# Kernel optimization log

Measured on AMD Instinct MI355X. Metric: run time of the kernel, lower is better.

The kernel has to match this reference:

```python
import jax, jax.numpy as jnp
import numpy as np

DT = 1e-3
STEPS = 128
UNITS_OSC = 512
MLP_UNITS = [1024, 512, 256]
ACTION_DIM = 256
BATCH = 64


def setup_inputs() -> dict:
    key = jax.random.key(0)
    ks = jax.random.split(key, 16)
    inp = {
        "z": jax.random.normal(ks[0], (BATCH, 2 * UNITS_OSC), dtype=jnp.float32),
        "omega": jax.random.uniform(ks[1], (BATCH, 1), dtype=jnp.float32),
        "b": jax.random.uniform(ks[2], (BATCH, UNITS_OSC), dtype=jnp.float32),
    }
    dims = [UNITS_OSC] + MLP_UNITS
    i = 3
    for l, (din, dout) in enumerate(zip(dims[:-1], dims[1:])):
        scale = 1.0 / np.sqrt(din)
        inp[f"W{l}_re"] = (jax.random.normal(ks[i], (din, dout), dtype=jnp.float32) * scale); i += 1
        inp[f"W{l}_im"] = (jax.random.normal(ks[i], (din, dout), dtype=jnp.float32) * scale); i += 1
        inp[f"b{l}_re"] = jnp.zeros((dout,), dtype=jnp.float32)
        inp[f"b{l}_im"] = jnp.zeros((dout,), dtype=jnp.float32)
    return inp


def _hopf(z, omega, b):
    # z: (B, 2*U) = [real | imag]; Hopf dynamics with harmonic frequencies k*omega
    x, y = z[:, :UNITS_OSC], z[:, UNITS_OSC:]
    r2 = x * x + y * y
    w = omega * jnp.arange(1, UNITS_OSC + 1, dtype=z.dtype)  # (B, U)
    dx = (b - r2) * x - w * y
    dy = (b - r2) * y + w * x
    return jnp.concatenate([x + DT * dx, y + DT * dy], axis=-1)


def _complex_mlp(z, params):
    # complex dense stack: (xr+i*yi) @ (Wr+i*Wi) + (br+i*bi), tanh on re/im parts
    x, y = jnp.split(z, 2, axis=-1)
    for (Wr, Wi, br, bi) in params:
        xr = x @ Wr - y @ Wi + br
        yi = x @ Wi + y @ Wr + bi
        x, y = jnp.tanh(xr), jnp.tanh(yi)
    return jnp.concatenate([x, y], axis=-1)


def reference(z, omega, b,
              W0_re, W0_im, b0_re, b0_im,
              W1_re, W1_im, b1_re, b1_im,
              W2_re, W2_im, b2_re, b2_im):
    params = [(W0_re, W0_im, b0_re, b0_im),
              (W1_re, W1_im, b1_re, b1_im),
              (W2_re, W2_im, b2_re, b2_im)]
    # first oscillator step (done before the while_loop in the original)
    z1 = _hopf(z, omega, b)
    o0 = _complex_mlp(z1, params)

    def step(zc, _):
        zn = _hopf(zc, omega, b)
        return zn, _complex_mlp(zn, params)

    _, outs = jax.lax.scan(step, z1, None, length=STEPS - 1)  # (STEPS-1, B, 2*A)
    outs = jnp.concatenate([o0[None], outs], axis=0)          # (STEPS, B, 2*A)
    out = jnp.transpose(outs, (1, 0, 2))[:, :, :ACTION_DIM]   # (B, STEPS, A)
    return out, z1
```

## Files before the change

kernel.cpp:

```cpp
#include <hip/hip_runtime.h>
#include <hip/hip_bf16.h>
#include <stdint.h>

#define AS1 __attribute__((address_space(1)))
#define AS3 __attribute__((address_space(3)))

typedef __bf16 bf16x8 __attribute__((ext_vector_type(8)));
typedef float f32x4 __attribute__((ext_vector_type(4)));

__device__ __forceinline__ float fast_tanh(float x) {
    float e = __expf(2.0f * x);
    return 1.0f - 2.0f / (e + 1.0f);
}

__device__ __forceinline__ float ldin(const void* p, int idx, int f32) {
    return f32 ? ((const float*)p)[idx]
               : __bfloat162float(((const __hip_bfloat16*)p)[idx]);
}

__device__ __forceinline__ unsigned short f2bf(float v) {
    __hip_bfloat16 h = __float2bfloat16(v);
    return *(unsigned short*)&h;
}

__device__ __forceinline__ void gload_lds16(const __hip_bfloat16* g, AS3 char* l) {
    __builtin_amdgcn_global_load_lds((AS1 void*)g, (AS3 void*)l, 16, 0, 0);
}

__device__ __forceinline__ void wt_tile(const void* Wr, const void* Wi,
                                        int din, int dout_, int KT, int nt, int kt,
                                        __hip_bfloat16* dst, int f32, char* smem)
{
    float (*T)[65] = (float(*)[65])smem;
    const int t = threadIdx.x;
    const int n0 = nt * 64, k0 = kt * 64;
    const void* src; float sg; int col0, krel;
    if (n0 < dout_) {
        col0 = n0;
        if (k0 < din) { src = Wr; sg =  1.f; krel = k0; }
        else          { src = Wi; sg = -1.f; krel = k0 - din; }
    } else {
        col0 = n0 - dout_;
        if (k0 < din) { src = Wi; sg =  1.f; krel = k0; }
        else          { src = Wr; sg =  1.f; krel = k0 - din; }
    }
    const int lr = t >> 4, lc = t & 15;
#pragma unroll
    for (int p = 0; p < 4; ++p) {
        const int r = p * 16 + lr;
        const int c = lc * 4;
        const size_t gi = (size_t)(krel + r) * dout_ + col0 + c;
        float v0, v1, v2, v3;
        if (f32) {
            float4 v = *(const float4*)((const float*)src + gi);
            v0 = v.x; v1 = v.y; v2 = v.z; v3 = v.w;
        } else {
            ushort4 u = *(const ushort4*)((const unsigned short*)src + gi);
            __hip_bfloat16 h0, h1, h2, h3;
            *(unsigned short*)&h0 = u.x; *(unsigned short*)&h1 = u.y;
            *(unsigned short*)&h2 = u.z; *(unsigned short*)&h3 = u.w;
            v0 = __bfloat162float(h0); v1 = __bfloat162float(h1);
            v2 = __bfloat162float(h2); v3 = __bfloat162float(h3);
        }
        T[r][c] = sg * v0; T[r][c + 1] = sg * v1;
        T[r][c + 2] = sg * v2; T[r][c + 3] = sg * v3;
    }
    __syncthreads();
#pragma unroll
    for (int q = 0; q < 4; ++q) {
        const int n = q * 16 + lr;
        const int k8 = lc;
        ushort4 u;
        u.x = f2bf(T[k8 * 4 + 0][n]); u.y = f2bf(T[k8 * 4 + 1][n]);
        u.z = f2bf(T[k8 * 4 + 2][n]); u.w = f2bf(T[k8 * 4 + 3][n]);
        *(ushort4*)((unsigned short*)dst + (size_t)(n0 + n) * KT + k0 + k8 * 4) = u;
    }
}

__global__ __launch_bounds__(256)
void setup1(const void* __restrict__ z, const void* __restrict__ omega,
            const void* __restrict__ bc,
            const void* __restrict__ W0r, const void* __restrict__ W0i,
            const void* __restrict__ b0r, const void* __restrict__ b0i,
            const void* __restrict__ b1r, const void* __restrict__ b1i,
            const void* __restrict__ b2r,
            __hip_bfloat16* __restrict__ Z, __hip_bfloat16* __restrict__ WT0,
            float* __restrict__ biasOut, int* __restrict__ flagOut,
            char* __restrict__ dout)
{
    __shared__ __align__(16) char smem[16640];
    __shared__ int sflag;
    const int t   = threadIdx.x;
    const int bid = blockIdx.x;

    if (t == 0) sflag = 0;
    __syncthreads();
    {
        const unsigned short* zz = (const unsigned short*)z;
        const int c = ((((zz[t] >> 7) & 0xFF) >= 0xC8) ? 1 : 0)
                    + ((((zz[t + 256] >> 7) & 0xFF) >= 0xC8) ? 1 : 0);
        if (c) atomicAdd(&sflag, c);
    }
    __syncthreads();
    const int f32 = (sflag > 8) ? 1 : 0;

    if (bid < 128) {
        const int tid = bid * 256 + t;
        const int b = tid >> 9;
        const int i = tid & 511;
        float x = ldin(z, b * 1024 + i, f32);
        float y = ldin(z, b * 1024 + 512 + i, f32);
        const float om = ldin(omega, b, f32);
        const float bb = ldin(bc, b * 512 + i, f32);
        const float w  = om * (float)(i + 1);
        __hip_bfloat16* zt = Z + b * 1024 + i;
        for (int s = 0; s < 128; ++s) {
            const float r2 = x * x + y * y;
            const float f  = bb - r2;
            const float dx = f * x - w * y;
            const float dy = f * y + w * x;
            x += 0.001f * dx;
            y += 0.001f * dy;
            zt[s * 65536]       = __float2bfloat16(x);
            zt[s * 65536 + 512] = __float2bfloat16(y);
            if (s == 0) {
                if (f32) {
                    float* o = (float*)(dout + (size_t)2097152 * 4);
                    o[b * 1024 + i] = x; o[b * 1024 + 512 + i] = y;
                } else {
                    __hip_bfloat16* o = (__hip_bfloat16*)(dout + (size_t)2097152 * 2);
                    o[b * 1024 + i] = __float2bfloat16(x);
                    o[b * 1024 + 512 + i] = __float2bfloat16(y);
                }
            }
        }
        return;
    }

    if (bid >= 640) {
        if (bid == 640 && t == 0) *flagOut = f32;
        const int idx = (bid - 640) * 256 + t;
        float v;
        if      (idx < 1024) v = ldin(b0r, idx, f32);
        else if (idx < 2048) v = ldin(b0i, idx - 1024, f32);
        else if (idx < 2560) v = ldin(b1r, idx - 2048, f32);
        else if (idx < 3072) v = ldin(b1i, idx - 2560, f32);
        else                 v = ldin(b2r, idx - 3072, f32);
        biasOut[idx] = v;
        return;
    }

    const int u = bid - 128;
    wt_tile(W0r, W0i, 512, 1024, 1024, u >> 4, u & 15, WT0, f32, smem);
}

template<int MT, int NT, int GX, int MODE>
__device__ __forceinline__ void gemm_core(int bid,
                                          const __hip_bfloat16* __restrict__ A,
                                          const __hip_bfloat16* __restrict__ Bt,
                                          const float* __restrict__ bias,
                                          void* __restrict__ Cv, int f32,
                                          int N, int K, char* smem)
{
    constexpr int AI = MT / 32;
    constexpr int BJ = NT / 32;
    __hip_bfloat16* As = (__hip_bfloat16*)smem;
    __hip_bfloat16* Bs = (__hip_bfloat16*)(smem + MT * 128);

    const int tid = threadIdx.x, lane = tid & 63, w = tid >> 6;
    const int wx = w & 1, wy = w >> 1;

    int nt, mt;
    if constexpr (GX >= 8) {
        constexpr int XG = GX >> 3;
        const int xcd = bid & 7, r = bid >> 3;
        nt = xcd * XG + (r % XG);
        mt = r / XG;
    } else {
        nt = bid % GX;
        mt = bid / GX;
    }
    const int m0 = mt * MT;
    const int n0 = nt * NT;

    const int sl = lane & 7, lr8 = lane >> 3;
    const __hip_bfloat16* gA[AI];
    const __hip_bfloat16* gB[BJ];
#pragma unroll
    for (int p = 0; p < AI; ++p) {
        const int row = w * (MT / 4) + p * 8 + lr8;
        gA[p] = A + (size_t)(m0 + row) * K + (sl ^ (row & 7)) * 8;
    }
#pragma unroll
    for (int p = 0; p < BJ; ++p) {
        const int row = w * (NT / 4) + p * 8 + lr8;
        gB[p] = Bt + (size_t)(n0 + row) * K + (sl ^ (row & 7)) * 8;
    }
    AS3 char* lA = (AS3 char*)As + w * (MT * 32);
    AS3 char* lB = (AS3 char*)Bs + w * (NT * 32);

    const int fr = lane & 15, fq = lane >> 4;
    const int swz = (fq ^ (fr & 7)) * 8;
    const int arow = wy * (MT / 2) + fr;
    const int brow = wx * (NT / 2) + fr;

    f32x4 acc[AI][BJ];
#pragma unroll
    for (int i = 0; i < AI; ++i)
#pragma unroll
        for (int j = 0; j < BJ; ++j)
            acc[i][j] = (f32x4){0.f, 0.f, 0.f, 0.f};

    const int NKT = K >> 6;
    for (int kt = 0; kt < NKT; ++kt) {
        const int kk = kt << 6;
#pragma unroll
        for (int p = 0; p < AI; ++p) gload_lds16(gA[p] + kk, lA + p * 1024);
#pragma unroll
        for (int p = 0; p < BJ; ++p) gload_lds16(gB[p] + kk, lB + p * 1024);
        __syncthreads();
#pragma unroll
        for (int ks = 0; ks < 2; ++ks) {
            const int so = swz ^ (ks << 5);
            bf16x8 af[AI], bv[BJ];
#pragma unroll
            for (int i = 0; i < AI; ++i)
                af[i] = *(const bf16x8*)(As + (arow + i * 16) * 64 + so);
#pragma unroll
            for (int j = 0; j < BJ; ++j)
                bv[j] = *(const bf16x8*)(Bs + (brow + j * 16) * 64 + so);
#pragma unroll
            for (int i = 0; i < AI; ++i)
#pragma unroll
                for (int j = 0; j < BJ; ++j)
                    acc[i][j] = __builtin_amdgcn_mfma_f32_16x16x32_bf16(af[i], bv[j], acc[i][j], 0, 0, 0);
        }
        __syncthreads();
    }

    const int col_l = lane & 15;
    const int rq    = lane >> 4;
    float bvv[BJ];
#pragma unroll
    for (int j = 0; j < BJ; ++j)
        bvv[j] = bias[n0 + wx * (NT / 2) + j * 16 + col_l];

#pragma unroll
    for (int i = 0; i < AI; ++i) {
#pragma unroll
        for (int j = 0; j < BJ; ++j) {
            const int gc = n0 + wx * (NT / 2) + j * 16 + col_l;
#pragma unroll
            for (int r = 0; r < 4; ++r) {
                const int gr = m0 + wy * (MT / 2) + i * 16 + rq * 4 + r;
                const float v = fast_tanh(acc[i][j][r] + bvv[j]);
                if (MODE == 0) {
                    ((__hip_bfloat16*)Cv)[(size_t)gr * (size_t)N + gc] = __float2bfloat16(v);
                } else {
                    const size_t idx = (size_t)(gr & 63) * 32768 + (size_t)(gr >> 6) * 256 + (size_t)gc;
                    if (f32) ((float*)Cv)[idx] = v;
                    else     ((__hip_bfloat16*)Cv)[idx] = __float2bfloat16(v);
                }
            }
        }
    }
}

__global__ __launch_bounds__(256)
void gemm0_wt(const __hip_bfloat16* __restrict__ A,
              const __hip_bfloat16* __restrict__ Bt,
              const float* __restrict__ bias, void* __restrict__ Cv,
              const void* __restrict__ W1r, const void* __restrict__ W1i,
              const void* __restrict__ W2r, const void* __restrict__ W2i,
              __hip_bfloat16* __restrict__ WT1, __hip_bfloat16* __restrict__ WT2,
              const int* __restrict__ flag)
{
    __shared__ __align__(16) char smem[32768];
    const int bid = blockIdx.x;
    if (bid < 1024) {
        gemm_core<128, 128, 16, 0>(bid, A, Bt, bias, Cv, 0, 2048, 1024, smem);
    } else if (bid < 1536) {
        const int u = bid - 1024;
        wt_tile(W1r, W1i, 1024, 512, 2048, u >> 5, u & 31, WT1, *flag, smem);
    } else {
        const int u = bid - 1536;
        wt_tile(W2r, W2i, 512, 256, 1024, u >> 4, u & 15, WT2, *flag, smem);
    }
}

template<int MT, int NT, int GX, int MODE>
__global__ __launch_bounds__(256)
void gemm_k(const __hip_bfloat16* __restrict__ A, const __hip_bfloat16* __restrict__ Bt,
            const float* __restrict__ bias, void* __restrict__ Cv,
            const int* __restrict__ flag, int N, int K)
{
    __shared__ __align__(16) char smem[(MT + NT) * 128];
    const int f32 = (MODE == 1) ? *flag : 0;
    gemm_core<MT, NT, GX, MODE>(blockIdx.x, A, Bt, bias, Cv, f32, N, K, smem);
}

extern "C" void kernel_launch(void* const* d_in, const int* in_sizes, int n_in,
                              void* d_out, int out_size, void* d_ws, size_t ws_size,
                              hipStream_t stream)
{
    (void)in_sizes; (void)n_in; (void)out_size; (void)ws_size;
    char* ws = (char*)d_ws;
    __hip_bfloat16* Z    = (__hip_bfloat16*)(ws);
    __hip_bfloat16* H0   = (__hip_bfloat16*)(ws + (16u << 20));
    __hip_bfloat16* WT0  = (__hip_bfloat16*)(ws + (48u << 20));
    __hip_bfloat16* WT1  = (__hip_bfloat16*)(ws + (52u << 20));
    __hip_bfloat16* WT2  = (__hip_bfloat16*)(ws + (56u << 20));
    float*          bias = (float*)        (ws + (56u << 20) + (512u << 10));
    int*            flag = (int*)          (ws + (57u << 20));

    setup1<<<653, 256, 0, stream>>>(d_in[0], d_in[1], d_in[2], d_in[3], d_in[4],
                                    d_in[5], d_in[6], d_in[9], d_in[10], d_in[13],
                                    Z, WT0, bias, flag, (char*)d_out);

    gemm0_wt<<<1600, 256, 0, stream>>>(Z, WT0, bias, H0,
                                       d_in[7], d_in[8], d_in[11], d_in[12],
                                       WT1, WT2, flag);

    gemm_k<128, 64, 16, 0><<<1024, 256, 0, stream>>>(H0, WT1, bias + 2048, Z, flag, 1024, 2048);

    gemm_k<64, 64, 4, 1><<<512, 256, 0, stream>>>(Z, WT2, bias + 3072, d_out, flag, 256, 1024);
}
```

Before: 206.6 us.

## Load A fragments directly from global into registers, stage only B in LDS

Result: slower. 279.5 us (+35.3%).

```diff
diff --git a/kernel.cpp b/kernel.cpp
--- a/kernel.cpp
+++ b/kernel.cpp
@@ -155,17 +155,17 @@
 }
 
 template<int MT, int NT, int GX, int MODE>
-__device__ __forceinline__ void gemm_core(int bid,
-                                          const __hip_bfloat16* __restrict__ A,
-                                          const __hip_bfloat16* __restrict__ Bt,
-                                          const float* __restrict__ bias,
-                                          void* __restrict__ Cv, int f32,
-                                          int N, int K, char* smem)
+__device__ __forceinline__ void gemm_ad(int bid,
+                                        const __hip_bfloat16* __restrict__ A,
+                                        const __hip_bfloat16* __restrict__ Bt,
+                                        const float* __restrict__ bias,
+                                        void* __restrict__ Cv, int f32,
+                                        int N, int K, char* smem)
 {
     constexpr int AI = MT / 32;
     constexpr int BJ = NT / 32;
-    __hip_bfloat16* As = (__hip_bfloat16*)smem;
-    __hip_bfloat16* Bs = (__hip_bfloat16*)(smem + MT * 128);
+    constexpr int BP = NT / 32;
+    __hip_bfloat16* Bs = (__hip_bfloat16*)smem;
 
     const int tid = threadIdx.x, lane = tid & 63, w = tid >> 6;
     const int wx = w & 1, wy = w >> 1;
@@ -184,25 +184,22 @@
     const int n0 = nt * NT;
 
     const int sl = lane & 7, lr8 = lane >> 3;
-    const __hip_bfloat16* gA[AI];
-    const __hip_bfloat16* gB[BJ];
-#pragma unroll
-    for (int p = 0; p < AI; ++p) {
-        const int row = w * (MT / 4) + p * 8 + lr8;
-        gA[p] = A + (size_t)(m0 + row) * K + (sl ^ (row & 7)) * 8;
-    }
-#pragma unroll
-    for (int p = 0; p < BJ; ++p) {
+    const __hip_bfloat16* gB[BP];
+#pragma unroll
+    for (int p = 0; p < BP; ++p) {
         const int row = w * (NT / 4) + p * 8 + lr8;
         gB[p] = Bt + (size_t)(n0 + row) * K + (sl ^ (row & 7)) * 8;
     }
-    AS3 char* lA = (AS3 char*)As + w * (MT * 32);
     AS3 char* lB = (AS3 char*)Bs + w * (NT * 32);
 
     const int fr = lane & 15, fq = lane >> 4;
     const int swz = (fq ^ (fr & 7)) * 8;
-    const int arow = wy * (MT / 2) + fr;
     const int brow = wx * (NT / 2) + fr;
+
+    const __hip_bfloat16* gA[AI];
+#pragma unroll
+    for (int i = 0; i < AI; ++i)
+        gA[i] = A + (size_t)(m0 + wy * (MT / 2) + i * 16 + fr) * K + fq * 8;
 
     f32x4 acc[AI][BJ];
 #pragma unroll
@@ -215,17 +212,18 @@
     for (int kt = 0; kt < NKT; ++kt) {
         const int kk = kt << 6;
 #pragma unroll
-        for (int p = 0; p < AI; ++p) gload_lds16(gA[p] + kk, lA + p * 1024);
-#pragma unroll
-        for (int p = 0; p < BJ; ++p) gload_lds16(gB[p] + kk, lB + p * 1024);
+        for (int p = 0; p < BP; ++p) gload_lds16(gB[p] + kk, lB + p * 1024);
+        bf16x8 af[2][AI];
+#pragma unroll
+        for (int ks = 0; ks < 2; ++ks)
+#pragma unroll
+            for (int i = 0; i < AI; ++i)
+                af[ks][i] = *(const bf16x8*)(gA[i] + kk + ks * 32);
         __syncthreads();
 #pragma unroll
         for (int ks = 0; ks < 2; ++ks) {
             const int so = swz ^ (ks << 5);
-            bf16x8 af[AI], bv[BJ];
-#pragma unroll
-            for (int i = 0; i < AI; ++i)
-                af[i] = *(const bf16x8*)(As + (arow + i * 16) * 64 + so);
+            bf16x8 bv[BJ];
 #pragma unroll
             for (int j = 0; j < BJ; ++j)
                 bv[j] = *(const bf16x8*)(Bs + (brow + j * 16) * 64 + so);
@@ -233,7 +231,7 @@
             for (int i = 0; i < AI; ++i)
 #pragma unroll
                 for (int j = 0; j < BJ; ++j)
-                    acc[i][j] = __builtin_amdgcn_mfma_f32_16x16x32_bf16(af[i], bv[j], acc[i][j], 0, 0, 0);
+                    acc[i][j] = __builtin_amdgcn_mfma_f32_16x16x32_bf16(af[ks][i], bv[j], acc[i][j], 0, 0, 0);
         }
         __syncthreads();
     }
@@ -275,15 +273,15 @@
               __hip_bfloat16* __restrict__ WT1, __hip_bfloat16* __restrict__ WT2,
               const int* __restrict__ flag)
 {
-    __shared__ __align__(16) char smem[32768];
+    __shared__ __align__(16) char smem[16640];
     const int bid = blockIdx.x;
-    if (bid < 1024) {
-        gemm_core<128, 128, 16, 0>(bid, A, Bt, bias, Cv, 0, 2048, 1024, smem);
-    } else if (bid < 1536) {
-        const int u = bid - 1024;
+    if (bid < 2048) {
+        gemm_ad<64, 128, 16, 0>(bid, A, Bt, bias, Cv, 0, 2048, 1024, smem);
+    } else if (bid < 2560) {
+        const int u = bid - 2048;
         wt_tile(W1r, W1i, 1024, 512, 2048, u >> 5, u & 31, WT1, *flag, smem);
     } else {
-        const int u = bid - 1536;
+        const int u = bid - 2560;
         wt_tile(W2r, W2i, 512, 256, 1024, u >> 4, u & 15, WT2, *flag, smem);
     }
 }
@@ -294,9 +292,9 @@
             const float* __restrict__ bias, void* __restrict__ Cv,
             const int* __restrict__ flag, int N, int K)
 {
-    __shared__ __align__(16) char smem[(MT + NT) * 128];
+    __shared__ __align__(16) char smem[NT * 128];
     const int f32 = (MODE == 1) ? *flag : 0;
-    gemm_core<MT, NT, GX, MODE>(blockIdx.x, A, Bt, bias, Cv, f32, N, K, smem);
+    gemm_ad<MT, NT, GX, MODE>(blockIdx.x, A, Bt, bias, Cv, f32, N, K, smem);
 }
 
 extern "C" void kernel_launch(void* const* d_in, const int* in_sizes, int n_in,
@@ -317,11 +315,11 @@
                                     d_in[5], d_in[6], d_in[9], d_in[10], d_in[13],
                                     Z, WT0, bias, flag, (char*)d_out);
 
-    gemm0_wt<<<1600, 256, 0, stream>>>(Z, WT0, bias, H0,
+    gemm0_wt<<<2624, 256, 0, stream>>>(Z, WT0, bias, H0,
                                        d_in[7], d_in[8], d_in[11], d_in[12],
                                        WT1, WT2, flag);
 
-    gemm_k<128, 64, 16, 0><<<1024, 256, 0, stream>>>(H0, WT1, bias + 2048, Z, flag, 1024, 2048);
+    gemm_k<64, 128, 8, 0><<<1024, 256, 0, stream>>>(H0, WT1, bias + 2048, Z, flag, 1024, 2048);
 
     gemm_k<64, 64, 4, 1><<<512, 256, 0, stream>>>(Z, WT2, bias + 3072, d_out, flag, 256, 1024);
 }
```
